# Kernel tuning notes

Measured on AMD Instinct MI355X. Metric: run time of the kernel, lower is better.

## Reference

```python
import jax, jax.numpy as jnp
import numpy as np

B, T, F, H, HEAD = 8192, 168, 64, 50, 100


def setup_inputs() -> dict:
    key = jax.random.key(0)
    ks = jax.random.split(key, 6)
    scale = lambda k, shape, fan: (jax.random.normal(k, shape, jnp.float32) / np.sqrt(fan)).astype(jnp.float32)
    x = jax.random.normal(ks[0], (B, T, F), jnp.float32)
    Wx = scale(ks[1], (F, 4 * H), F)          # input->gates [i,f,g,o]
    Wh = scale(ks[2], (H, 4 * H), H)          # hidden->gates
    b = jnp.zeros((4 * H,), jnp.float32).at[H:2 * H].set(1.0)  # unit_forget_bias
    W1 = scale(ks[3], (H, HEAD), H)
    b1 = jnp.zeros((HEAD,), jnp.float32)
    W2 = scale(ks[4], (HEAD, 1), HEAD)
    b2 = jnp.zeros((1,), jnp.float32)
    return {"x": x, "Wx": Wx, "Wh": Wh, "b": b, "W1": W1, "b1": b1, "W2": W2, "b2": b2}


def reference(x, Wx, Wh, b, W1, b1, W2, b2):
    # x: [B, T, F]. Unrolled LSTM (Keras LSTMCell: sigmoid gates, tanh activation),
    # take last hidden state, MLP head, residual add of last-step feature 0.
    Bn = x.shape[0]
    Hn = Wh.shape[0]
    h0 = jnp.zeros((Bn, Hn), x.dtype)
    c0 = jnp.zeros((Bn, Hn), x.dtype)

    def step(carry, xt):
        h, c = carry
        z = xt @ Wx + h @ Wh + b           # [B, 4H]
        i, f, g, o = jnp.split(z, 4, axis=-1)
        c = jax.nn.sigmoid(f) * c + jax.nn.sigmoid(i) * jnp.tanh(g)
        h = jax.nn.sigmoid(o) * jnp.tanh(c)
        return (h, c), None

    xs = jnp.swapaxes(x, 0, 1)             # [T, B, F]
    (h_last, _), _ = jax.lax.scan(step, (h0, c0), xs)
    out = jax.nn.relu(h_last @ W1 + b1) @ W2 + b2   # [B, 1]
    return out + x[:, -1, 0:1]
```

## Files before the change

kernel.cpp:

```cpp
#include <hip/hip_runtime.h>


#define B_N 8192
#define T_N 168
#define F_N 64
#define H_N 50
#define HEAD_N 100
#define ROWSTRIDE (T_N * F_N)

typedef _Float16 f16x8 __attribute__((ext_vector_type(8)));
typedef _Float16 f16x4 __attribute__((ext_vector_type(4)));
typedef float    f32x4 __attribute__((ext_vector_type(4)));

#define LOG2E  1.4426950408889634f
#define LOG2E2 2.8853900817779268f

#define MFMA __builtin_amdgcn_mfma_f32_16x16x32_f16

#define BAR()                                                        \
    do {                                                             \
        asm volatile("s_waitcnt lgkmcnt(0)" ::: "memory");           \
        __builtin_amdgcn_s_barrier();                                \
        asm volatile("" ::: "memory");                               \
    } while (0)

__device__ __forceinline__ float rcp_f(float v) { return __builtin_amdgcn_rcpf(v); }
#if __has_builtin(__builtin_amdgcn_exp2f)
__device__ __forceinline__ float exp2_f(float v) { return __builtin_amdgcn_exp2f(v); }
#else
__device__ __forceinline__ float exp2_f(float v) { return __expf(0.6931471805599453f * v); }
#endif

__launch_bounds__(512, 4)
__global__ void lstm_fused(const float* __restrict__ x,
                           const float* __restrict__ Wx,
                           const float* __restrict__ Wh,
                           const float* __restrict__ b,
                           const float* __restrict__ W1,
                           const float* __restrict__ b1,
                           const float* __restrict__ W2,
                           const float* __restrict__ b2,
                           float* __restrict__ out)
{
    __shared__ alignas(16) _Float16 xb[2][16][72];
    __shared__ alignas(16) _Float16 hb[2][16][72];
    __shared__ alignas(16) float axb[2][4][4][64][4];
    __shared__ float hrelu[16][HEAD_N];

    const int tid  = threadIdx.x;
    const int lane = tid & 63;
    const int w    = tid >> 6;
    const int ut   = w & 3;
    const int rowA = lane & 15;
    const int kg   = lane >> 4;
    const int R0   = blockIdx.x * 16;
    const int jl   = ut * 16 + rowA;
    const bool jv  = (jl < H_N);

    f16x8 wxf[4][2], whf[4][2];
    float bg[4];
    if (w < 4) {
        #pragma unroll
        for (int g = 0; g < 4; ++g) {
            const float sc = (g == 2) ? LOG2E2 : LOG2E;
            bg[g] = jv ? b[g * H_N + jl] * sc : 0.0f;
            #pragma unroll
            for (int ks = 0; ks < 2; ++ks) {
                f16x8 v;
                #pragma unroll
                for (int i = 0; i < 8; ++i) {
                    int k = ks * 32 + kg * 8 + i;
                    v[i] = (_Float16)(jv ? Wx[k * 200 + g * H_N + jl] * sc : 0.0f);
                }
                wxf[g][ks] = v;
            }
        }
    } else {
        #pragma unroll
        for (int g = 0; g < 4; ++g) {
            const float sc = (g == 2) ? LOG2E2 : LOG2E;
            #pragma unroll
            for (int ks = 0; ks < 2; ++ks) {
                f16x8 v;
                #pragma unroll
                for (int i = 0; i < 8; ++i) {
                    int k = ks * 32 + kg * 8 + i;
                    v[i] = (_Float16)((jv && k < H_N) ? Wh[k * 200 + g * H_N + jl] * sc : 0.0f);
                }
                whf[g][ks] = v;
            }
        }
    }

    float c0 = 0.f, c1 = 0.f, c2 = 0.f, c3 = 0.f;

    for (int idx = tid; idx < 16 * 72; idx += 512)
        ((_Float16*)hb[0])[idx] = (_Float16)0.0f;

    const int xr  = (tid >> 4) & 15;
    const int xf0 = (tid & 15) * 4;
    const float* xrow = x + (size_t)(R0 + xr) * ROWSTRIDE + xf0;
    f32x4 xpr0, xpr1;
    if (w < 4) {
        f32x4 v0 = *reinterpret_cast<const f32x4*>(xrow);
        f32x4 v1 = *reinterpret_cast<const f32x4*>(xrow + F_N);
        xpr0 = *reinterpret_cast<const f32x4*>(xrow + 2 * F_N);
        xpr1 = *reinterpret_cast<const f32x4*>(xrow + 3 * F_N);
        f16x4 a, c4;
        #pragma unroll
        for (int j = 0; j < 4; ++j) { a[j] = (_Float16)v0[j]; c4[j] = (_Float16)v1[j]; }
        *reinterpret_cast<f16x4*>(&xb[0][xr][xf0]) = a;
        *reinterpret_cast<f16x4*>(&xb[1][xr][xf0]) = c4;
    }
    const float* xld = xrow + 4 * F_N;
    __syncthreads();

    if (w < 4) {
        f16x8 xa0 = *reinterpret_cast<const f16x8*>(&xb[0][rowA][kg * 8]);
        f16x8 xa1 = *reinterpret_cast<const f16x8*>(&xb[0][rowA][32 + kg * 8]);
        f32x4 a0 = {bg[0], bg[0], bg[0], bg[0]};
        f32x4 a1 = {bg[1], bg[1], bg[1], bg[1]};
        f32x4 a2 = {bg[2], bg[2], bg[2], bg[2]};
        f32x4 a3 = {bg[3], bg[3], bg[3], bg[3]};
        a0 = MFMA(xa0, wxf[0][0], a0, 0, 0, 0);
        a1 = MFMA(xa0, wxf[1][0], a1, 0, 0, 0);
        a2 = MFMA(xa0, wxf[2][0], a2, 0, 0, 0);
        a3 = MFMA(xa0, wxf[3][0], a3, 0, 0, 0);
        a0 = MFMA(xa1, wxf[0][1], a0, 0, 0, 0);
        a1 = MFMA(xa1, wxf[1][1], a1, 0, 0, 0);
        a2 = MFMA(xa1, wxf[2][1], a2, 0, 0, 0);
        a3 = MFMA(xa1, wxf[3][1], a3, 0, 0, 0);
        *reinterpret_cast<f32x4*>(&axb[0][ut][0][lane][0]) = a0;
        *reinterpret_cast<f32x4*>(&axb[0][ut][1][lane][0]) = a1;
        *reinterpret_cast<f32x4*>(&axb[0][ut][2][lane][0]) = a2;
        *reinterpret_cast<f32x4*>(&axb[0][ut][3][lane][0]) = a3;
    }
    __syncthreads();

#define GATE1(PW, ii, cvar)                                                    \
    {                                                                          \
        float A_ = exp2_f(-zi[ii]);                                            \
        float B_ = exp2_f(-zg[ii]);                                            \
        float F_ = exp2_f(-zf[ii]);                                            \
        float sf_ = rcp_f(1.0f + F_);                                          \
        float r1_ = rcp_f((1.0f + A_) * (1.0f + B_));                          \
        float cn_ = fmaf(sf_, cvar, (1.0f - B_) * r1_);                        \
        cvar = cn_;                                                            \
        float C_ = exp2_f(-zo[ii]);                                            \
        float eD_ = fminf(-LOG2E2 * cn_, 80.0f);                               \
        float D_ = exp2_f(eD_);                                                \
        float r2_ = rcp_f((1.0f + C_) * (1.0f + D_));                          \
        hb[PW][kg * 4 + ii][jl] = (_Float16)((1.0f - D_) * r2_);               \
    }

#define XSTEP(P, DO_XW, DO_LOAD)                                               \
    {                                                                          \
        f16x8 xa0 = *reinterpret_cast<const f16x8*>(&xb[P ^ 1][rowA][kg * 8]);      \
        f16x8 xa1 = *reinterpret_cast<const f16x8*>(&xb[P ^ 1][rowA][32 + kg * 8]); \
        f32x4 a0 = {bg[0], bg[0], bg[0], bg[0]};                               \
        f32x4 a1 = {bg[1], bg[1], bg[1], bg[1]};                               \
        f32x4 a2 = {bg[2], bg[2], bg[2], bg[2]};                               \
        f32x4 a3 = {bg[3], bg[3], bg[3], bg[3]};                               \
        a0 = MFMA(xa0, wxf[0][0], a0, 0, 0, 0);                                \
        a1 = MFMA(xa0, wxf[1][0], a1, 0, 0, 0);                                \
        a2 = MFMA(xa0, wxf[2][0], a2, 0, 0, 0);                                \
        a3 = MFMA(xa0, wxf[3][0], a3, 0, 0, 0);                                \
        a0 = MFMA(xa1, wxf[0][1], a0, 0, 0, 0);                                \
        a1 = MFMA(xa1, wxf[1][1], a1, 0, 0, 0);                                \
        a2 = MFMA(xa1, wxf[2][1], a2, 0, 0, 0);                                \
        a3 = MFMA(xa1, wxf[3][1], a3, 0, 0, 0);                                \
        *reinterpret_cast<f32x4*>(&axb[P ^ 1][ut][0][lane][0]) = a0;           \
        *reinterpret_cast<f32x4*>(&axb[P ^ 1][ut][1][lane][0]) = a1;           \
        *reinterpret_cast<f32x4*>(&axb[P ^ 1][ut][2][lane][0]) = a2;           \
        *reinterpret_cast<f32x4*>(&axb[P ^ 1][ut][3][lane][0]) = a3;           \
        if (DO_XW) {                                                           \
            f16x4 xc;                                                          \
            xc[0] = (_Float16)xpr##P[0]; xc[1] = (_Float16)xpr##P[1];          \
            xc[2] = (_Float16)xpr##P[2]; xc[3] = (_Float16)xpr##P[3];          \
            *reinterpret_cast<f16x4*>(&xb[P][xr][xf0]) = xc;                   \
        }                                                                      \
        if (DO_LOAD) { xpr##P = *reinterpret_cast<const f32x4*>(xld); xld += F_N; } \
        BAR();                                                                 \
    }

#define HSTEP(P)                                                               \
    {                                                                          \
        __builtin_amdgcn_s_setprio(1);                                         \
        f16x8 ha0 = *reinterpret_cast<const f16x8*>(&hb[P][rowA][kg * 8]);     \
        f16x8 ha1 = *reinterpret_cast<const f16x8*>(&hb[P][rowA][32 + kg * 8]);\
        f32x4 zi = *reinterpret_cast<const f32x4*>(&axb[P][ut][0][lane][0]);   \
        f32x4 zf = *reinterpret_cast<const f32x4*>(&axb[P][ut][1][lane][0]);   \
        f32x4 zg = *reinterpret_cast<const f32x4*>(&axb[P][ut][2][lane][0]);   \
        f32x4 zo = *reinterpret_cast<const f32x4*>(&axb[P][ut][3][lane][0]);   \
        zi = MFMA(ha0, whf[0][0], zi, 0, 0, 0);                                \
        zf = MFMA(ha0, whf[1][0], zf, 0, 0, 0);                                \
        zg = MFMA(ha0, whf[2][0], zg, 0, 0, 0);                                \
        zo = MFMA(ha0, whf[3][0], zo, 0, 0, 0);                                \
        zi = MFMA(ha1, whf[0][1], zi, 0, 0, 0);                                \
        zf = MFMA(ha1, whf[1][1], zf, 0, 0, 0);                                \
        zg = MFMA(ha1, whf[2][1], zg, 0, 0, 0);                                \
        zo = MFMA(ha1, whf[3][1], zo, 0, 0, 0);                                \
        GATE1(P ^ 1, 0, c0)                                                    \
        GATE1(P ^ 1, 1, c1)                                                    \
        GATE1(P ^ 1, 2, c2)                                                    \
        GATE1(P ^ 1, 3, c3)                                                    \
        __builtin_amdgcn_s_setprio(0);                                         \
        BAR();                                                                 \
    }

    if (w < 4) {
        for (int it = 0; it < 82; ++it) {
            XSTEP(0, 1, 1)
            XSTEP(1, 1, 1)
        }
        XSTEP(0, 1, 0)
        XSTEP(1, 1, 0)
        XSTEP(0, 0, 0)
        BAR();
    } else {
        for (int it = 0; it < 82; ++it) {
            HSTEP(0)
            HSTEP(1)
        }
        HSTEP(0)
        HSTEP(1)
        HSTEP(0)
        HSTEP(1)
    }
#undef XSTEP
#undef HSTEP
#undef GATE1

    if (tid < 256) {
        const int r1 = tid & 15;
        const int u1 = tid >> 4;
        float hrow[H_N];
        #pragma unroll
        for (int k = 0; k < H_N; ++k) hrow[k] = (float)hb[0][r1][k];
        for (int uu = u1; uu < HEAD_N; uu += 16) {
            float s = b1[uu];
            #pragma unroll
            for (int k = 0; k < H_N; ++k) s += hrow[k] * W1[k * HEAD_N + uu];
            hrelu[r1][uu] = fmaxf(s, 0.0f);
        }
    }
    __syncthreads();
    if (tid < 256) {
        const int r2 = tid >> 4;
        const int p  = tid & 15;
        float s = 0.0f;
        for (int uu = p; uu < HEAD_N; uu += 16) s += hrelu[r2][uu] * W2[uu];
        #pragma unroll
        for (int off = 8; off > 0; off >>= 1) s += __shfl_xor(s, off, 16);
        if (p == 0) {
            float res = x[(size_t)(R0 + r2) * ROWSTRIDE + (T_N - 1) * F_N + 0];
            out[R0 + r2] = s + b2[0] + res;
        }
    }
}

extern "C" void kernel_launch(void* const* d_in, const int* in_sizes, int n_in,
                              void* d_out, int out_size, void* d_ws, size_t ws_size,
                              hipStream_t stream) {
    const float* x  = (const float*)d_in[0];
    const float* Wx = (const float*)d_in[1];
    const float* Wh = (const float*)d_in[2];
    const float* b  = (const float*)d_in[3];
    const float* W1 = (const float*)d_in[4];
    const float* b1 = (const float*)d_in[5];
    const float* W2 = (const float*)d_in[6];
    const float* b2 = (const float*)d_in[7];
    float* out = (float*)d_out;

    lstm_fused<<<dim3(B_N / 16), dim3(512), 0, stream>>>(x, Wx, Wh, b, W1, b1, W2, b2, out);
}
```

Measured before the change: 151.7 us.

## Interleave two independent 16-row batch groups per block to hide recurrence latency

Each block now processes 32 batch rows as two independent 16-row LSTM groups. The h-warps alternate between the groups each barrier window, so one group's MFMA and gate latency overlaps the other's. The gate output is held in registers and written to LDS one window later. Launch bounds drop to 2 blocks per CU and there are half as many blocks, which trades occupancy and parallelism for more instruction-level overlap. The step is also split into twice as many, shorter barrier windows.

```diff
diff --git a/kernel.cpp b/kernel.cpp
--- a/kernel.cpp
+++ b/kernel.cpp
@@ -31,7 +31,7 @@
 __device__ __forceinline__ float exp2_f(float v) { return __expf(0.6931471805599453f * v); }
 #endif
 
-__launch_bounds__(512, 4)
+__launch_bounds__(512, 2)
 __global__ void lstm_fused(const float* __restrict__ x,
                            const float* __restrict__ Wx,
                            const float* __restrict__ Wh,
@@ -42,10 +42,9 @@
                            const float* __restrict__ b2,
                            float* __restrict__ out)
 {
-    __shared__ alignas(16) _Float16 xb[2][16][72];
-    __shared__ alignas(16) _Float16 hb[2][16][72];
-    __shared__ alignas(16) float axb[2][4][4][64][4];
-    __shared__ float hrelu[16][HEAD_N];
+    __shared__ alignas(16) _Float16 xb[2][2][16][72];
+    __shared__ alignas(16) _Float16 hb[2][2][16][72];
+    __shared__ alignas(16) float    axb[2][2][4][4][64][4];
 
     const int tid  = threadIdx.x;
     const int lane = tid & 63;
@@ -53,13 +52,18 @@
     const int ut   = w & 3;
     const int rowA = lane & 15;
     const int kg   = lane >> 4;
-    const int R0   = blockIdx.x * 16;
+    const int R0   = blockIdx.x * 32;
     const int jl   = ut * 16 + rowA;
     const bool jv  = (jl < H_N);
 
-    f16x8 wxf[4][2], whf[4][2];
-    float bg[4];
+    for (int idx = tid; idx < 16 * 72; idx += 512) {
+        ((_Float16*)hb[0][0])[idx] = (_Float16)0.0f;
+        ((_Float16*)hb[1][0])[idx] = (_Float16)0.0f;
+    }
+
     if (w < 4) {
+        f16x8 wxf[4][2];
+        float bg[4];
         #pragma unroll
         for (int g = 0; g < 4; ++g) {
             const float sc = (g == 2) ? LOG2E2 : LOG2E;
@@ -75,7 +79,120 @@
                 wxf[g][ks] = v;
             }
         }
+
+        const int xr  = (tid >> 4) & 15;
+        const int xf0 = (tid & 15) * 4;
+        const float* xrowA = x + (size_t)(R0 + xr) * ROWSTRIDE + xf0;
+        const float* xrowB = x + (size_t)(R0 + 16 + xr) * ROWSTRIDE + xf0;
+        f32x4 xprA0, xprA1, xprB0, xprB1;
+        {
+            f32x4 a0 = *reinterpret_cast<const f32x4*>(xrowA);
+            f32x4 a1 = *reinterpret_cast<const f32x4*>(xrowA + F_N);
+            xprA0 = *reinterpret_cast<const f32x4*>(xrowA + 2 * F_N);
+            xprA1 = *reinterpret_cast<const f32x4*>(xrowA + 3 * F_N);
+            f32x4 b0 = *reinterpret_cast<const f32x4*>(xrowB);
+            f32x4 b1v = *reinterpret_cast<const f32x4*>(xrowB + F_N);
+            xprB0 = *reinterpret_cast<const f32x4*>(xrowB + 2 * F_N);
+            xprB1 = *reinterpret_cast<const f32x4*>(xrowB + 3 * F_N);
+            f16x4 c0, c1, c2, c3;
+            #pragma unroll
+            for (int j = 0; j < 4; ++j) {
+                c0[j] = (_Float16)a0[j]; c1[j] = (_Float16)a1[j];
+                c2[j] = (_Float16)b0[j]; c3[j] = (_Float16)b1v[j];
+            }
+            *reinterpret_cast<f16x4*>(&xb[0][0][xr][xf0]) = c0;
+            *reinterpret_cast<f16x4*>(&xb[0][1][xr][xf0]) = c1;
+            *reinterpret_cast<f16x4*>(&xb[1][0][xr][xf0]) = c2;
+            *reinterpret_cast<f16x4*>(&xb[1][1][xr][xf0]) = c3;
+        }
+        const float* xldA = xrowA + 4 * F_N;
+        const float* xldB = xrowB + 4 * F_N;
+        BAR();
+
+        #pragma unroll
+        for (int G = 0; G < 2; ++G) {
+            f16x8 xa0 = *reinterpret_cast<const f16x8*>(&xb[G][0][rowA][kg * 8]);
+            f16x8 xa1 = *reinterpret_cast<const f16x8*>(&xb[G][0][rowA][32 + kg * 8]);
+            f32x4 a0 = {bg[0], bg[0], bg[0], bg[0]};
+            f32x4 a1 = {bg[1], bg[1], bg[1], bg[1]};
+            f32x4 a2 = {bg[2], bg[2], bg[2], bg[2]};
+            f32x4 a3 = {bg[3], bg[3], bg[3], bg[3]};
+            a0 = MFMA(xa0, wxf[0][0], a0, 0, 0, 0);
+            a1 = MFMA(xa0, wxf[1][0], a1, 0, 0, 0);
+            a2 = MFMA(xa0, wxf[2][0], a2, 0, 0, 0);
+            a3 = MFMA(xa0, wxf[3][0], a3, 0, 0, 0);
+            a0 = MFMA(xa1, wxf[0][1], a0, 0, 0, 0);
+            a1 = MFMA(xa1, wxf[1][1], a1, 0, 0, 0);
+            a2 = MFMA(xa1, wxf[2][1], a2, 0, 0, 0);
+            a3 = MFMA(xa1, wxf[3][1], a3, 0, 0, 0);
+            *reinterpret_cast<f32x4*>(&axb[G][0][ut][0][lane][0]) = a0;
+            *reinterpret_cast<f32x4*>(&axb[G][0][ut][1][lane][0]) = a1;
+            *reinterpret_cast<f32x4*>(&axb[G][0][ut][2][lane][0]) = a2;
+            *reinterpret_cast<f32x4*>(&axb[G][0][ut][3][lane][0]) = a3;
+        }
+        BAR();
+
+        f32x4 pax0, pax1, pax2, pax3;
+
+#define XWIN(G, RB, FLUSH, FG, FB, DO_XW, WB, XPR, DO_LOAD, XLD)               \
+    {                                                                          \
+        f16x8 xa0 = *reinterpret_cast<const f16x8*>(&xb[G][RB][rowA][kg * 8]); \
+        f16x8 xa1 = *reinterpret_cast<const f16x8*>(&xb[G][RB][rowA][32 + kg * 8]); \
+        if (FLUSH) {                                                           \
+            *reinterpret_cast<f32x4*>(&axb[FG][FB][ut][0][lane][0]) = pax0;    \
+            *reinterpret_cast<f32x4*>(&axb[FG][FB][ut][1][lane][0]) = pax1;    \
+            *reinterpret_cast<f32x4*>(&axb[FG][FB][ut][2][lane][0]) = pax2;    \
+            *reinterpret_cast<f32x4*>(&axb[FG][FB][ut][3][lane][0]) = pax3;    \
+        }                                                                      \
+        pax0 = (f32x4){bg[0], bg[0], bg[0], bg[0]};                            \
+        pax1 = (f32x4){bg[1], bg[1], bg[1], bg[1]};                            \
+        pax2 = (f32x4){bg[2], bg[2], bg[2], bg[2]};                            \
+        pax3 = (f32x4){bg[3], bg[3], bg[3], bg[3]};                            \
+        pax0 = MFMA(xa0, wxf[0][0], pax0, 0, 0, 0);                            \
+        pax1 = MFMA(xa0, wxf[1][0], pax1, 0, 0, 0);                            \
+        pax2 = MFMA(xa0, wxf[2][0], pax2, 0, 0, 0);                            \
+        pax3 = MFMA(xa0, wxf[3][0], pax3, 0, 0, 0);                            \
+        pax0 = MFMA(xa1, wxf[0][1], pax0, 0, 0, 0);                            \
+        pax1 = MFMA(xa1, wxf[1][1], pax1, 0, 0, 0);                            \
+        pax2 = MFMA(xa1, wxf[2][1], pax2, 0, 0, 0);                            \
+        pax3 = MFMA(xa1, wxf[3][1], pax3, 0, 0, 0);                            \
+        if (DO_XW) {                                                           \
+            f16x4 xc;                                                          \
+            xc[0] = (_Float16)XPR[0]; xc[1] = (_Float16)XPR[1];                \
+            xc[2] = (_Float16)XPR[2]; xc[3] = (_Float16)XPR[3];                \
+            *reinterpret_cast<f16x4*>(&xb[G][WB][xr][xf0]) = xc;               \
+        }                                                                      \
+        if (DO_LOAD) { XPR = *reinterpret_cast<const f32x4*>(XLD); XLD += F_N; } \
+        BAR();                                                                 \
+    }
+
+        XWIN(0, 1, 0, 0, 0, 1, 0, xprA0, 1, xldA)
+        XWIN(1, 1, 1, 0, 1, 1, 0, xprB0, 1, xldB)
+        XWIN(0, 0, 1, 1, 1, 1, 1, xprA1, 1, xldA)
+        XWIN(1, 0, 1, 0, 0, 1, 1, xprB1, 1, xldB)
+        for (int it = 1; it < 82; ++it) {
+            XWIN(0, 1, 1, 1, 0, 1, 0, xprA0, 1, xldA)
+            XWIN(1, 1, 1, 0, 1, 1, 0, xprB0, 1, xldB)
+            XWIN(0, 0, 1, 1, 1, 1, 1, xprA1, 1, xldA)
+            XWIN(1, 0, 1, 0, 0, 1, 1, xprB1, 1, xldB)
+        }
+        XWIN(0, 1, 1, 1, 0, 1, 0, xprA0, 0, xldA)
+        XWIN(1, 1, 1, 0, 1, 1, 0, xprB0, 0, xldB)
+        XWIN(0, 0, 1, 1, 1, 1, 1, xprA1, 0, xldA)
+        XWIN(1, 0, 1, 0, 0, 1, 1, xprB1, 0, xldB)
+        XWIN(0, 1, 1, 1, 0, 0, 0, xprA0, 0, xldA)
+        XWIN(1, 1, 1, 0, 1, 0, 0, xprB0, 0, xldB)
+        {
+            *reinterpret_cast<f32x4*>(&axb[1][1][ut][0][lane][0]) = pax0;
+            *reinterpret_cast<f32x4*>(&axb[1][1][ut][1][lane][0]) = pax1;
+            *reinterpret_cast<f32x4*>(&axb[1][1][ut][2][lane][0]) = pax2;
+            *reinterpret_cast<f32x4*>(&axb[1][1][ut][3][lane][0]) = pax3;
+            BAR();
+        }
+        BAR();
+#undef XWIN
     } else {
+        f16x8 whf[4][2];
         #pragma unroll
         for (int g = 0; g < 4; ++g) {
             const float sc = (g == 2) ? LOG2E2 : LOG2E;
@@ -90,59 +207,19 @@
                 whf[g][ks] = v;
             }
         }
-    }
-
-    float c0 = 0.f, c1 = 0.f, c2 = 0.f, c3 = 0.f;
-
-    for (int idx = tid; idx < 16 * 72; idx += 512)
-        ((_Float16*)hb[0])[idx] = (_Float16)0.0f;
-
-    const int xr  = (tid >> 4) & 15;
-    const int xf0 = (tid & 15) * 4;
-    const float* xrow = x + (size_t)(R0 + xr) * ROWSTRIDE + xf0;
-    f32x4 xpr0, xpr1;
-    if (w < 4) {
-        f32x4 v0 = *reinterpret_cast<const f32x4*>(xrow);
-        f32x4 v1 = *reinterpret_cast<const f32x4*>(xrow + F_N);
-        xpr0 = *reinterpret_cast<const f32x4*>(xrow + 2 * F_N);
-        xpr1 = *reinterpret_cast<const f32x4*>(xrow + 3 * F_N);
-        f16x4 a, c4;
-        #pragma unroll
-        for (int j = 0; j < 4; ++j) { a[j] = (_Float16)v0[j]; c4[j] = (_Float16)v1[j]; }
-        *reinterpret_cast<f16x4*>(&xb[0][xr][xf0]) = a;
-        *reinterpret_cast<f16x4*>(&xb[1][xr][xf0]) = c4;
-    }
-    const float* xld = xrow + 4 * F_N;
-    __syncthreads();
-
-    if (w < 4) {
-        f16x8 xa0 = *reinterpret_cast<const f16x8*>(&xb[0][rowA][kg * 8]);
-        f16x8 xa1 = *reinterpret_cast<const f16x8*>(&xb[0][rowA][32 + kg * 8]);
-        f32x4 a0 = {bg[0], bg[0], bg[0], bg[0]};
-        f32x4 a1 = {bg[1], bg[1], bg[1], bg[1]};
-        f32x4 a2 = {bg[2], bg[2], bg[2], bg[2]};
-        f32x4 a3 = {bg[3], bg[3], bg[3], bg[3]};
-        a0 = MFMA(xa0, wxf[0][0], a0, 0, 0, 0);
-        a1 = MFMA(xa0, wxf[1][0], a1, 0, 0, 0);
-        a2 = MFMA(xa0, wxf[2][0], a2, 0, 0, 0);
-        a3 = MFMA(xa0, wxf[3][0], a3, 0, 0, 0);
-        a0 = MFMA(xa1, wxf[0][1], a0, 0, 0, 0);
-        a1 = MFMA(xa1, wxf[1][1], a1, 0, 0, 0);
-        a2 = MFMA(xa1, wxf[2][1], a2, 0, 0, 0);
-        a3 = MFMA(xa1, wxf[3][1], a3, 0, 0, 0);
-        *reinterpret_cast<f32x4*>(&axb[0][ut][0][lane][0]) = a0;
-        *reinterpret_cast<f32x4*>(&axb[0][ut][1][lane][0]) = a1;
-        *reinterpret_cast<f32x4*>(&axb[0][ut][2][lane][0]) = a2;
-        *reinterpret_cast<f32x4*>(&axb[0][ut][3][lane][0]) = a3;
-    }
-    __syncthreads();
-
-#define GATE1(PW, ii, cvar)                                                    \
+        float cA0 = 0.f, cA1 = 0.f, cA2 = 0.f, cA3 = 0.f;
+        float cB0 = 0.f, cB1 = 0.f, cB2 = 0.f, cB3 = 0.f;
+        f16x4 ph;
+
+        BAR();
+        BAR();
+
+#define GATE1(ii, cvar)                                                        \
     {                                                                          \
         float A_ = exp2_f(-zi[ii]);                                            \
         float B_ = exp2_f(-zg[ii]);                                            \
-        float F_ = exp2_f(-zf[ii]);                                            \
-        float sf_ = rcp_f(1.0f + F_);                                          \
+        float E_ = exp2_f(-zf[ii]);                                            \
+        float sf_ = rcp_f(1.0f + E_);                                          \
         float r1_ = rcp_f((1.0f + A_) * (1.0f + B_));                          \
         float cn_ = fmaf(sf_, cvar, (1.0f - B_) * r1_);                        \
         cvar = cn_;                                                            \
@@ -150,48 +227,24 @@
         float eD_ = fminf(-LOG2E2 * cn_, 80.0f);                               \
         float D_ = exp2_f(eD_);                                                \
         float r2_ = rcp_f((1.0f + C_) * (1.0f + D_));                          \
-        hb[PW][kg * 4 + ii][jl] = (_Float16)((1.0f - D_) * r2_);               \
-    }
-
-#define XSTEP(P, DO_XW, DO_LOAD)                                               \
-    {                                                                          \
-        f16x8 xa0 = *reinterpret_cast<const f16x8*>(&xb[P ^ 1][rowA][kg * 8]);      \
-        f16x8 xa1 = *reinterpret_cast<const f16x8*>(&xb[P ^ 1][rowA][32 + kg * 8]); \
-        f32x4 a0 = {bg[0], bg[0], bg[0], bg[0]};                               \
-        f32x4 a1 = {bg[1], bg[1], bg[1], bg[1]};                               \
-        f32x4 a2 = {bg[2], bg[2], bg[2], bg[2]};                               \
-        f32x4 a3 = {bg[3], bg[3], bg[3], bg[3]};                               \
-        a0 = MFMA(xa0, wxf[0][0], a0, 0, 0, 0);                                \
-        a1 = MFMA(xa0, wxf[1][0], a1, 0, 0, 0);                                \
-        a2 = MFMA(xa0, wxf[2][0], a2, 0, 0, 0);                                \
-        a3 = MFMA(xa0, wxf[3][0], a3, 0, 0, 0);                                \
-        a0 = MFMA(xa1, wxf[0][1], a0, 0, 0, 0);                                \
-        a1 = MFMA(xa1, wxf[1][1], a1, 0, 0, 0);                                \
-        a2 = MFMA(xa1, wxf[2][1], a2, 0, 0, 0);                                \
-        a3 = MFMA(xa1, wxf[3][1], a3, 0, 0, 0);                                \
-        *reinterpret_cast<f32x4*>(&axb[P ^ 1][ut][0][lane][0]) = a0;           \
-        *reinterpret_cast<f32x4*>(&axb[P ^ 1][ut][1][lane][0]) = a1;           \
-        *reinterpret_cast<f32x4*>(&axb[P ^ 1][ut][2][lane][0]) = a2;           \
-        *reinterpret_cast<f32x4*>(&axb[P ^ 1][ut][3][lane][0]) = a3;           \
-        if (DO_XW) {                                                           \
-            f16x4 xc;                                                          \
-            xc[0] = (_Float16)xpr##P[0]; xc[1] = (_Float16)xpr##P[1];          \
-            xc[2] = (_Float16)xpr##P[2]; xc[3] = (_Float16)xpr##P[3];          \
-            *reinterpret_cast<f16x4*>(&xb[P][xr][xf0]) = xc;                   \
-        }                                                                      \
-        if (DO_LOAD) { xpr##P = *reinterpret_cast<const f32x4*>(xld); xld += F_N; } \
-        BAR();                                                                 \
-    }
-
-#define HSTEP(P)                                                               \
+        ph[ii] = (_Float16)((1.0f - D_) * r2_);                                \
+    }
+
+#define HWIN(G, RB, FLUSH, FG, FB, C0, C1, C2, C3)                             \
     {                                                                          \
         __builtin_amdgcn_s_setprio(1);                                         \
-        f16x8 ha0 = *reinterpret_cast<const f16x8*>(&hb[P][rowA][kg * 8]);     \
-        f16x8 ha1 = *reinterpret_cast<const f16x8*>(&hb[P][rowA][32 + kg * 8]);\
-        f32x4 zi = *reinterpret_cast<const f32x4*>(&axb[P][ut][0][lane][0]);   \
-        f32x4 zf = *reinterpret_cast<const f32x4*>(&axb[P][ut][1][lane][0]);   \
-        f32x4 zg = *reinterpret_cast<const f32x4*>(&axb[P][ut][2][lane][0]);   \
-        f32x4 zo = *reinterpret_cast<const f32x4*>(&axb[P][ut][3][lane][0]);   \
+        f16x8 ha0 = *reinterpret_cast<const f16x8*>(&hb[G][RB][rowA][kg * 8]); \
+        f16x8 ha1 = *reinterpret_cast<const f16x8*>(&hb[G][RB][rowA][32 + kg * 8]); \
+        f32x4 zi = *reinterpret_cast<const f32x4*>(&axb[G][RB][ut][0][lane][0]); \
+        f32x4 zf = *reinterpret_cast<const f32x4*>(&axb[G][RB][ut][1][lane][0]); \
+        f32x4 zg = *reinterpret_cast<const f32x4*>(&axb[G][RB][ut][2][lane][0]); \
+        f32x4 zo = *reinterpret_cast<const f32x4*>(&axb[G][RB][ut][3][lane][0]); \
+        if (FLUSH) {                                                           \
+            hb[FG][FB][kg * 4 + 0][jl] = ph[0];                                \
+            hb[FG][FB][kg * 4 + 1][jl] = ph[1];                                \
+            hb[FG][FB][kg * 4 + 2][jl] = ph[2];                                \
+            hb[FG][FB][kg * 4 + 3][jl] = ph[3];                                \
+        }                                                                      \
         zi = MFMA(ha0, whf[0][0], zi, 0, 0, 0);                                \
         zf = MFMA(ha0, whf[1][0], zf, 0, 0, 0);                                \
         zg = MFMA(ha0, whf[2][0], zg, 0, 0, 0);                                \
@@ -200,43 +253,40 @@
         zf = MFMA(ha1, whf[1][1], zf, 0, 0, 0);                                \
         zg = MFMA(ha1, whf[2][1], zg, 0, 0, 0);                                \
         zo = MFMA(ha1, whf[3][1], zo, 0, 0, 0);                                \
-        GATE1(P ^ 1, 0, c0)                                                    \
-        GATE1(P ^ 1, 1, c1)                                                    \
-        GATE1(P ^ 1, 2, c2)                                                    \
-        GATE1(P ^ 1, 3, c3)                                                    \
+        GATE1(0, C0)                                                           \
+        GATE1(1, C1)                                                           \
+        GATE1(2, C2)                                                           \
+        GATE1(3, C3)                                                           \
         __builtin_amdgcn_s_setprio(0);                                         \
         BAR();                                                                 \
     }
 
-    if (w < 4) {
-        for (int it = 0; it < 82; ++it) {
-            XSTEP(0, 1, 1)
-            XSTEP(1, 1, 1)
-        }
-        XSTEP(0, 1, 0)
-        XSTEP(1, 1, 0)
-        XSTEP(0, 0, 0)
-        BAR();
-    } else {
-        for (int it = 0; it < 82; ++it) {
-            HSTEP(0)
-            HSTEP(1)
-        }
-        HSTEP(0)
-        HSTEP(1)
-        HSTEP(0)
-        HSTEP(1)
-    }
-#undef XSTEP
-#undef HSTEP
+        HWIN(0, 0, 0, 0, 0, cA0, cA1, cA2, cA3)
+        HWIN(1, 0, 1, 0, 1, cB0, cB1, cB2, cB3)
+        HWIN(0, 1, 1, 1, 1, cA0, cA1, cA2, cA3)
+        HWIN(1, 1, 1, 0, 0, cB0, cB1, cB2, cB3)
+        for (int it = 1; it < 84; ++it) {
+            HWIN(0, 0, 1, 1, 0, cA0, cA1, cA2, cA3)
+            HWIN(1, 0, 1, 0, 1, cB0, cB1, cB2, cB3)
+            HWIN(0, 1, 1, 1, 1, cA0, cA1, cA2, cA3)
+            HWIN(1, 1, 1, 0, 0, cB0, cB1, cB2, cB3)
+        }
+        hb[1][0][kg * 4 + 0][jl] = ph[0];
+        hb[1][0][kg * 4 + 1][jl] = ph[1];
+        hb[1][0][kg * 4 + 2][jl] = ph[2];
+        hb[1][0][kg * 4 + 3][jl] = ph[3];
+#undef HWIN
 #undef GATE1
-
-    if (tid < 256) {
-        const int r1 = tid & 15;
-        const int u1 = tid >> 4;
+    }
+    __syncthreads();
+
+    float (*hrelu)[HEAD_N] = reinterpret_cast<float (*)[HEAD_N]>(&axb[0][0][0][0][0][0]);
+    {
+        const int r1 = tid & 31;
+        const int u1 = tid >> 5;
         float hrow[H_N];
         #pragma unroll
-        for (int k = 0; k < H_N; ++k) hrow[k] = (float)hb[0][r1][k];
+        for (int k = 0; k < H_N; ++k) hrow[k] = (float)hb[r1 >> 4][0][r1 & 15][k];
         for (int uu = u1; uu < HEAD_N; uu += 16) {
             float s = b1[uu];
             #pragma unroll
@@ -245,7 +295,7 @@
         }
     }
     __syncthreads();
-    if (tid < 256) {
+    {
         const int r2 = tid >> 4;
         const int p  = tid & 15;
         float s = 0.0f;
@@ -272,5 +322,5 @@
     const float* b2 = (const float*)d_in[7];
     float* out = (float*)d_out;
 
-    lstm_fused<<<dim3(B_N / 16), dim3(512), 0, stream>>>(x, Wx, Wh, b, W1, b1, W2, b2, out);
+    lstm_fused<<<dim3(B_N / 32), dim3(512), 0, stream>>>(x, Wx, Wh, b, W1, b1, W2, b2, out);
 }
```

After: 164.8 us. 1.09x slower.

## Load x directly into MFMA fragments and store input projections as fp16

Applied to the files above, without the earlier changes.

Producer waves now load x rows straight from global memory in MFMA operand layout, converting to fp16 in registers. This removes the LDS staging buffer for x and its extra write/read per step. The precomputed input projections exchanged through LDS are also stored as fp16 instead of fp32, halving LDS traffic and footprint, with consumer waves converting them back to fp32 before accumulating. This costs some precision on the pre-activation gate values and more global load instructions per producer lane, each a less-coalesced 8-float chunk.

```diff
diff --git a/kernel.cpp b/kernel.cpp
--- a/kernel.cpp
+++ b/kernel.cpp
@@ -30,6 +30,13 @@
 #else
 __device__ __forceinline__ float exp2_f(float v) { return __expf(0.6931471805599453f * v); }
 #endif
+
+__device__ __forceinline__ f16x8 cvt8(f32x4 a, f32x4 b) {
+    f16x8 r;
+    #pragma unroll
+    for (int j = 0; j < 4; ++j) { r[j] = (_Float16)a[j]; r[4 + j] = (_Float16)b[j]; }
+    return r;
+}
 
 __launch_bounds__(512, 4)
 __global__ void lstm_fused(const float* __restrict__ x,
@@ -42,9 +49,8 @@
                            const float* __restrict__ b2,
                            float* __restrict__ out)
 {
-    __shared__ alignas(16) _Float16 xb[2][16][72];
     __shared__ alignas(16) _Float16 hb[2][16][72];
-    __shared__ alignas(16) float axb[2][4][4][64][4];
+    __shared__ alignas(16) _Float16 axbh[2][4][2][64][8];
     __shared__ float hrelu[16][HEAD_N];
 
     const int tid  = threadIdx.x;
@@ -97,27 +103,27 @@
     for (int idx = tid; idx < 16 * 72; idx += 512)
         ((_Float16*)hb[0])[idx] = (_Float16)0.0f;
 
-    const int xr  = (tid >> 4) & 15;
-    const int xf0 = (tid & 15) * 4;
-    const float* xrow = x + (size_t)(R0 + xr) * ROWSTRIDE + xf0;
-    f32x4 xpr0, xpr1;
+    const float* xbase = x + (size_t)(R0 + rowA) * ROWSTRIDE + kg * 8;
+    f32x4 xp0_0, xp0_1, xp0_2, xp0_3;
+    f32x4 xp1_0, xp1_1, xp1_2, xp1_3;
+    const float* xldf = xbase + 3 * F_N;
+
     if (w < 4) {
-        f32x4 v0 = *reinterpret_cast<const f32x4*>(xrow);
-        f32x4 v1 = *reinterpret_cast<const f32x4*>(xrow + F_N);
-        xpr0 = *reinterpret_cast<const f32x4*>(xrow + 2 * F_N);
-        xpr1 = *reinterpret_cast<const f32x4*>(xrow + 3 * F_N);
-        f16x4 a, c4;
-        #pragma unroll
-        for (int j = 0; j < 4; ++j) { a[j] = (_Float16)v0[j]; c4[j] = (_Float16)v1[j]; }
-        *reinterpret_cast<f16x4*>(&xb[0][xr][xf0]) = a;
-        *reinterpret_cast<f16x4*>(&xb[1][xr][xf0]) = c4;
-    }
-    const float* xld = xrow + 4 * F_N;
-    __syncthreads();
-
-    if (w < 4) {
-        f16x8 xa0 = *reinterpret_cast<const f16x8*>(&xb[0][rowA][kg * 8]);
-        f16x8 xa1 = *reinterpret_cast<const f16x8*>(&xb[0][rowA][32 + kg * 8]);
+        f32x4 t0 = *reinterpret_cast<const f32x4*>(xbase + 0);
+        f32x4 t1 = *reinterpret_cast<const f32x4*>(xbase + 4);
+        f32x4 t2 = *reinterpret_cast<const f32x4*>(xbase + 32);
+        f32x4 t3 = *reinterpret_cast<const f32x4*>(xbase + 36);
+        xp0_0 = *reinterpret_cast<const f32x4*>(xbase + F_N + 0);
+        xp0_1 = *reinterpret_cast<const f32x4*>(xbase + F_N + 4);
+        xp0_2 = *reinterpret_cast<const f32x4*>(xbase + F_N + 32);
+        xp0_3 = *reinterpret_cast<const f32x4*>(xbase + F_N + 36);
+        xp1_0 = *reinterpret_cast<const f32x4*>(xbase + 2 * F_N + 0);
+        xp1_1 = *reinterpret_cast<const f32x4*>(xbase + 2 * F_N + 4);
+        xp1_2 = *reinterpret_cast<const f32x4*>(xbase + 2 * F_N + 32);
+        xp1_3 = *reinterpret_cast<const f32x4*>(xbase + 2 * F_N + 36);
+
+        f16x8 xa0 = cvt8(t0, t1);
+        f16x8 xa1 = cvt8(t2, t3);
         f32x4 a0 = {bg[0], bg[0], bg[0], bg[0]};
         f32x4 a1 = {bg[1], bg[1], bg[1], bg[1]};
         f32x4 a2 = {bg[2], bg[2], bg[2], bg[2]};
@@ -130,10 +136,8 @@
         a1 = MFMA(xa1, wxf[1][1], a1, 0, 0, 0);
         a2 = MFMA(xa1, wxf[2][1], a2, 0, 0, 0);
         a3 = MFMA(xa1, wxf[3][1], a3, 0, 0, 0);
-        *reinterpret_cast<f32x4*>(&axb[0][ut][0][lane][0]) = a0;
-        *reinterpret_cast<f32x4*>(&axb[0][ut][1][lane][0]) = a1;
-        *reinterpret_cast<f32x4*>(&axb[0][ut][2][lane][0]) = a2;
-        *reinterpret_cast<f32x4*>(&axb[0][ut][3][lane][0]) = a3;
+        *reinterpret_cast<f16x8*>(&axbh[0][ut][0][lane][0]) = cvt8(a0, a1);
+        *reinterpret_cast<f16x8*>(&axbh[0][ut][1][lane][0]) = cvt8(a2, a3);
     }
     __syncthreads();
 
@@ -153,10 +157,10 @@
         hb[PW][kg * 4 + ii][jl] = (_Float16)((1.0f - D_) * r2_);               \
     }
 
-#define XSTEP(P, DO_XW, DO_LOAD)                                               \
+#define XSTEP(P, DO_LOAD)                                                      \
     {                                                                          \
-        f16x8 xa0 = *reinterpret_cast<const f16x8*>(&xb[P ^ 1][rowA][kg * 8]);      \
-        f16x8 xa1 = *reinterpret_cast<const f16x8*>(&xb[P ^ 1][rowA][32 + kg * 8]); \
+        f16x8 xa0 = cvt8(xp##P##_0, xp##P##_1);                                \
+        f16x8 xa1 = cvt8(xp##P##_2, xp##P##_3);                                \
         f32x4 a0 = {bg[0], bg[0], bg[0], bg[0]};                               \
         f32x4 a1 = {bg[1], bg[1], bg[1], bg[1]};                               \
         f32x4 a2 = {bg[2], bg[2], bg[2], bg[2]};                               \
@@ -169,17 +173,15 @@
         a1 = MFMA(xa1, wxf[1][1], a1, 0, 0, 0);                                \
         a2 = MFMA(xa1, wxf[2][1], a2, 0, 0, 0);                                \
         a3 = MFMA(xa1, wxf[3][1], a3, 0, 0, 0);                                \
-        *reinterpret_cast<f32x4*>(&axb[P ^ 1][ut][0][lane][0]) = a0;           \
-        *reinterpret_cast<f32x4*>(&axb[P ^ 1][ut][1][lane][0]) = a1;           \
-        *reinterpret_cast<f32x4*>(&axb[P ^ 1][ut][2][lane][0]) = a2;           \
-        *reinterpret_cast<f32x4*>(&axb[P ^ 1][ut][3][lane][0]) = a3;           \
-        if (DO_XW) {                                                           \
-            f16x4 xc;                                                          \
-            xc[0] = (_Float16)xpr##P[0]; xc[1] = (_Float16)xpr##P[1];          \
-            xc[2] = (_Float16)xpr##P[2]; xc[3] = (_Float16)xpr##P[3];          \
-            *reinterpret_cast<f16x4*>(&xb[P][xr][xf0]) = xc;                   \
+        *reinterpret_cast<f16x8*>(&axbh[P ^ 1][ut][0][lane][0]) = cvt8(a0, a1);\
+        *reinterpret_cast<f16x8*>(&axbh[P ^ 1][ut][1][lane][0]) = cvt8(a2, a3);\
+        if (DO_LOAD) {                                                         \
+            xp##P##_0 = *reinterpret_cast<const f32x4*>(xldf + 0);             \
+            xp##P##_1 = *reinterpret_cast<const f32x4*>(xldf + 4);             \
+            xp##P##_2 = *reinterpret_cast<const f32x4*>(xldf + 32);            \
+            xp##P##_3 = *reinterpret_cast<const f32x4*>(xldf + 36);            \
+            xldf += F_N;                                                       \
         }                                                                      \
-        if (DO_LOAD) { xpr##P = *reinterpret_cast<const f32x4*>(xld); xld += F_N; } \
         BAR();                                                                 \
     }
 
@@ -188,10 +190,14 @@
         __builtin_amdgcn_s_setprio(1);                                         \
         f16x8 ha0 = *reinterpret_cast<const f16x8*>(&hb[P][rowA][kg * 8]);     \
         f16x8 ha1 = *reinterpret_cast<const f16x8*>(&hb[P][rowA][32 + kg * 8]);\
-        f32x4 zi = *reinterpret_cast<const f32x4*>(&axb[P][ut][0][lane][0]);   \
-        f32x4 zf = *reinterpret_cast<const f32x4*>(&axb[P][ut][1][lane][0]);   \
-        f32x4 zg = *reinterpret_cast<const f32x4*>(&axb[P][ut][2][lane][0]);   \
-        f32x4 zo = *reinterpret_cast<const f32x4*>(&axb[P][ut][3][lane][0]);   \
+        f16x8 r0 = *reinterpret_cast<const f16x8*>(&axbh[P][ut][0][lane][0]);  \
+        f16x8 r1 = *reinterpret_cast<const f16x8*>(&axbh[P][ut][1][lane][0]);  \
+        f32x4 zi, zf, zg, zo;                                                  \
+        _Pragma("unroll")                                                      \
+        for (int j = 0; j < 4; ++j) {                                          \
+            zi[j] = (float)r0[j];  zf[j] = (float)r0[4 + j];                   \
+            zg[j] = (float)r1[j];  zo[j] = (float)r1[4 + j];                   \
+        }                                                                      \
         zi = MFMA(ha0, whf[0][0], zi, 0, 0, 0);                                \
         zf = MFMA(ha0, whf[1][0], zf, 0, 0, 0);                                \
         zg = MFMA(ha0, whf[2][0], zg, 0, 0, 0);                                \
@@ -210,12 +216,12 @@
 
     if (w < 4) {
         for (int it = 0; it < 82; ++it) {
-            XSTEP(0, 1, 1)
-            XSTEP(1, 1, 1)
-        }
-        XSTEP(0, 1, 0)
-        XSTEP(1, 1, 0)
-        XSTEP(0, 0, 0)
+            XSTEP(0, 1)
+            XSTEP(1, 1)
+        }
+        XSTEP(0, 1)
+        XSTEP(1, 0)
+        XSTEP(0, 0)
         BAR();
     } else {
         for (int it = 0; it < 82; ++it) {
```

Result: slower. 181.4 us (+19.6%).
